# Kernel tuning notes

Measured on AMD Instinct MI355X. Metric: run time of the kernel, lower is better.

Reference implementation:

```python
import jax, jax.numpy as jnp
import numpy as np

B, S, HID = 2, 2048, 3584
NH, NKV, HD = 16, 8, 256
EPS = 1e-6
SCALING = 256 ** (-0.5)  # query_pre_attn_scalar ** -0.5
NEG = -1e9


def setup_inputs() -> dict:
    key = jax.random.key(0)
    ks = jax.random.split(key, 8)
    hidden_states = jax.random.normal(ks[0], (B, S, HID), jnp.float32)
    # RoPE tables (theta=10000), shape [B, S, HD]
    inv_freq = 1.0 / (10000.0 ** (np.arange(0, HD, 2, dtype=np.float32) / HD))
    pos = np.arange(S, dtype=np.float32)
    freqs = np.outer(pos, inv_freq)                      # [S, HD/2]
    emb = np.concatenate([freqs, freqs], axis=-1)        # [S, HD]
    cos = jnp.broadcast_to(jnp.asarray(np.cos(emb)), (B, S, HD)).astype(jnp.float32)
    sin = jnp.broadcast_to(jnp.asarray(np.sin(emb)), (B, S, HD)).astype(jnp.float32)
    # additive causal mask [B,1,S,S]
    causal = jnp.where(jnp.tril(jnp.ones((S, S), bool)), 0.0, NEG).astype(jnp.float32)
    attention_mask = jnp.broadcast_to(causal[None, None], (B, 1, S, S))
    sc = 0.02
    Wq = jax.random.normal(ks[1], (NH * HD, HID), jnp.float32) * sc
    Wk = jax.random.normal(ks[2], (NKV * HD, HID), jnp.float32) * sc
    Wv = jax.random.normal(ks[3], (NKV * HD, HID), jnp.float32) * sc
    Wo = jax.random.normal(ks[4], (HID, NH * HD), jnp.float32) * sc
    q_norm_w = jax.random.normal(ks[5], (HD,), jnp.float32) * 0.1
    k_norm_w = jax.random.normal(ks[6], (HD,), jnp.float32) * 0.1
    return dict(hidden_states=hidden_states, cos=cos, sin=sin,
                attention_mask=attention_mask, Wq=Wq, Wk=Wk, Wv=Wv, Wo=Wo,
                q_norm_w=q_norm_w, k_norm_w=k_norm_w)


def _rmsnorm(x, w, eps=EPS):
    # out = x * rsqrt(mean(x^2)) * (1 + w)
    xf = x.astype(jnp.float32)
    out = xf * jax.lax.rsqrt(jnp.mean(xf * xf, axis=-1, keepdims=True) + eps)
    return (out * (1.0 + w.astype(jnp.float32))).astype(x.dtype)


def _rotate_half(x):
    d = x.shape[-1] // 2
    return jnp.concatenate([-x[..., d:], x[..., :d]], axis=-1)


def reference(hidden_states, cos, sin, attention_mask, Wq, Wk, Wv, Wo, q_norm_w, k_norm_w):
    b, s, _ = hidden_states.shape
    # projections -> [B, H, S, D]
    q = jnp.einsum('bsh,dh->bsd', hidden_states, Wq).reshape(b, s, NH, HD).transpose(0, 2, 1, 3)
    k = jnp.einsum('bsh,dh->bsd', hidden_states, Wk).reshape(b, s, NKV, HD).transpose(0, 2, 1, 3)
    v = jnp.einsum('bsh,dh->bsd', hidden_states, Wv).reshape(b, s, NKV, HD).transpose(0, 2, 1, 3)
    # per-head RMSNorm on Q/K
    q = _rmsnorm(q, q_norm_w)
    k = _rmsnorm(k, k_norm_w)
    # RoPE, cos/sin broadcast over head dim (unsqueeze_dim=1)
    c, sn = cos[:, None], sin[:, None]
    q = q * c + _rotate_half(q) * sn
    k = k * c + _rotate_half(k) * sn
    # GQA: repeat kv heads (n_rep = NH // NKV)
    n_rep = NH // NKV
    k = jnp.repeat(k, n_rep, axis=1)
    v = jnp.repeat(v, n_rep, axis=1)
    # scaled dot-product attention, softmax in fp32
    scores = jnp.einsum('bhqd,bhkd->bhqk', q, k) * SCALING
    scores = scores + attention_mask[:, :, :, :k.shape[2]]
    attn_weights = jax.nn.softmax(scores.astype(jnp.float32), axis=-1).astype(q.dtype)
    attn_out = jnp.einsum('bhqk,bhkd->bqhd', attn_weights, v).reshape(b, s, NH * HD)
    attn_out = jnp.einsum('bsd,hd->bsh', attn_out, Wo)
    return attn_out, attn_weights
```

## Files before the change

kernel.cpp:

```cpp
#include <hip/hip_runtime.h>

#define B_    2
#define S_    2048
#define HID_  3584
#define NH_   16
#define NKV_  8
#define HD_   256
#define DQ_   (NH_ * HD_)
#define DKV_  (NKV_ * HD_)

static constexpr float SCALE_ = 0.0625f;

typedef __bf16 bf16_t;
typedef __bf16 bf16x8 __attribute__((ext_vector_type(8)));
typedef __bf16 bf16x4 __attribute__((ext_vector_type(4)));
typedef float  f32x4  __attribute__((ext_vector_type(4)));

__global__ __launch_bounds__(256) void cvt_kernel(const float* __restrict__ in,
                                                  bf16_t* __restrict__ out, int n4) {
  int i = blockIdx.x * 256 + threadIdx.x;
  if (i < n4) {
    float4 v = ((const float4*)in)[i];
    bf16x4 o;
    o[0] = (bf16_t)v.x; o[1] = (bf16_t)v.y; o[2] = (bf16_t)v.z; o[3] = (bf16_t)v.w;
    ((bf16x4*)out)[i] = o;
  }
}

__device__ inline void gload_lds16(const bf16_t* g, bf16_t* l) {
  __builtin_amdgcn_global_load_lds(
      (const __attribute__((address_space(1))) void*)g,
      (__attribute__((address_space(3))) void*)l, 16, 0, 0);
}

template<int MODE>
__global__ __launch_bounds__(512, 1) void gemm256(const bf16_t* __restrict__ A,
                                                  const bf16_t* __restrict__ Bt,
                                                  void* __restrict__ outv,
                                                  void* __restrict__ out2v,
                                                  int M, int N, int K, int nh) {
  __shared__ __align__(16) bf16_t As[2][256 * 64];
  __shared__ __align__(16) bf16_t Bs[2][256 * 64];
  const int t = threadIdx.x;
  const int lane = t & 63, wv = t >> 6;
  const int wr = wv >> 2, wc = wv & 3;
  const int lr = lane & 15, lg = lane >> 4;
  const size_t m0 = (size_t)blockIdx.y * 256, n0 = (size_t)blockIdx.x * 256;

  const int srow = wv * 8 + (lane >> 3);
  const int scol = ((lane & 7) ^ ((lane >> 3) & 7)) * 8;
  const bf16_t* ga = A  + (m0 + srow) * (size_t)K + scol;
  const bf16_t* gb = Bt + (n0 + srow) * (size_t)K + scol;
  const int ldso = wv * 512;

#define SITEA(rb, kc, pp) gload_lds16(ga + (size_t)(rb) * K + (kc), &As[pp][(rb) * 64 + ldso])
#define SITEB(rb, kc, pp) gload_lds16(gb + (size_t)(rb) * K + (kc), &Bs[pp][(rb) * 64 + ldso])

  const int NT = K >> 6;
  f32x4 acc[8][4] = {};
  bf16x8 af[4][2], bfr[2][2];

  const int swz0 = ((0 + lg) ^ (lr & 7)) * 8;
  const int swz1 = ((4 + lg) ^ (lr & 7)) * 8;
  const int aRB = (wr * 128 + lr) * 64;
  const int bRB = (wc * 64 + lr) * 64;

  SITEA(0, 0, 0); SITEA(64, 0, 0); SITEA(128, 0, 0); SITEA(192, 0, 0);
  SITEB(0, 0, 0); SITEB(64, 0, 0); SITEB(128, 0, 0); SITEB(192, 0, 0);

  for (int kt = 0; kt < NT; ++kt) {
    const int p = kt & 1, q = p ^ 1;
    __syncthreads();
    if (kt + 1 < NT) {
      const int kn = (kt + 1) << 6;
      SITEA(0, kn, q); SITEA(64, kn, q); SITEA(128, kn, q); SITEA(192, kn, q);
      SITEB(0, kn, q); SITEB(64, kn, q); SITEB(128, kn, q); SITEB(192, kn, q);
    }

#pragma unroll
    for (int i = 0; i < 4; ++i) {
      af[i][0] = *(const bf16x8*)&As[p][aRB + i * 1024 + swz0];
      af[i][1] = *(const bf16x8*)&As[p][aRB + i * 1024 + swz1];
    }
#pragma unroll
    for (int j = 0; j < 2; ++j) {
      bfr[j][0] = *(const bf16x8*)&Bs[p][bRB + j * 1024 + swz0];
      bfr[j][1] = *(const bf16x8*)&Bs[p][bRB + j * 1024 + swz1];
    }
#pragma unroll
    for (int i = 0; i < 4; ++i)
#pragma unroll
      for (int j = 0; j < 2; ++j) {
        acc[i][j] = __builtin_amdgcn_mfma_f32_16x16x32_bf16(af[i][0], bfr[j][0], acc[i][j], 0, 0, 0);
        acc[i][j] = __builtin_amdgcn_mfma_f32_16x16x32_bf16(af[i][1], bfr[j][1], acc[i][j], 0, 0, 0);
      }

#pragma unroll
    for (int i = 0; i < 4; ++i) {
      af[i][0] = *(const bf16x8*)&As[p][aRB + (i + 4) * 1024 + swz0];
      af[i][1] = *(const bf16x8*)&As[p][aRB + (i + 4) * 1024 + swz1];
    }
#pragma unroll
    for (int i = 0; i < 4; ++i)
#pragma unroll
      for (int j = 0; j < 2; ++j) {
        acc[i + 4][j] = __builtin_amdgcn_mfma_f32_16x16x32_bf16(af[i][0], bfr[j][0], acc[i + 4][j], 0, 0, 0);
        acc[i + 4][j] = __builtin_amdgcn_mfma_f32_16x16x32_bf16(af[i][1], bfr[j][1], acc[i + 4][j], 0, 0, 0);
      }

#pragma unroll
    for (int j = 0; j < 2; ++j) {
      bfr[j][0] = *(const bf16x8*)&Bs[p][bRB + (j + 2) * 1024 + swz0];
      bfr[j][1] = *(const bf16x8*)&Bs[p][bRB + (j + 2) * 1024 + swz1];
    }
#pragma unroll
    for (int i = 0; i < 4; ++i)
#pragma unroll
      for (int j = 0; j < 2; ++j) {
        acc[i + 4][j + 2] = __builtin_amdgcn_mfma_f32_16x16x32_bf16(af[i][0], bfr[j][0], acc[i + 4][j + 2], 0, 0, 0);
        acc[i + 4][j + 2] = __builtin_amdgcn_mfma_f32_16x16x32_bf16(af[i][1], bfr[j][1], acc[i + 4][j + 2], 0, 0, 0);
      }

#pragma unroll
    for (int i = 0; i < 4; ++i) {
      af[i][0] = *(const bf16x8*)&As[p][aRB + i * 1024 + swz0];
      af[i][1] = *(const bf16x8*)&As[p][aRB + i * 1024 + swz1];
    }
#pragma unroll
    for (int i = 0; i < 4; ++i)
#pragma unroll
      for (int j = 0; j < 2; ++j) {
        acc[i][j + 2] = __builtin_amdgcn_mfma_f32_16x16x32_bf16(af[i][0], bfr[j][0], acc[i][j + 2], 0, 0, 0);
        acc[i][j + 2] = __builtin_amdgcn_mfma_f32_16x16x32_bf16(af[i][1], bfr[j][1], acc[i][j + 2], 0, 0, 0);
      }
  }
#undef SITEA
#undef SITEB

#pragma unroll
  for (int i = 0; i < 8; ++i)
#pragma unroll
    for (int j = 0; j < 4; ++j) {
      const int row0 = (int)m0 + wr * 128 + i * 16 + lg * 4;
      const int col  = (int)n0 + wc * 64 + j * 16 + lr;
#pragma unroll
      for (int r = 0; r < 4; ++r) {
        const int row = row0 + r;
        if (MODE == 0) {
          ((float*)outv)[(size_t)row * N + col] = acc[i][j][r];
        } else {
          const bf16_t val = (bf16_t)acc[i][j][r];
          const int b = row >> 11, s = row & (S_ - 1);
          if (MODE == 1) {
            const int h = col >> 8, hd = col & (HD_ - 1);
            ((bf16_t*)outv)[((size_t)(b * nh + h) * S_ + s) * HD_ + hd] = val;
          } else {
            if (col < DKV_) {
              const int h = col >> 8, hd = col & (HD_ - 1);
              ((bf16_t*)outv)[((size_t)(b * NKV_ + h) * S_ + s) * HD_ + hd] = val;
            } else {
              const int c2 = col - DKV_;
              const int h = c2 >> 8, hd = c2 & (HD_ - 1);
              ((bf16_t*)out2v)[((size_t)(b * NKV_ + h) * HD_ + hd) * S_ + s] = val;
            }
          }
        }
      }
    }
}

template<int LOGNH>
__global__ __launch_bounds__(256) void normrope_kernel(bf16_t* __restrict__ x,
                                                       const float* __restrict__ w,
                                                       const float* __restrict__ cosb,
                                                       const float* __restrict__ sinb,
                                                       float* __restrict__ rownorm) {
  const int gid  = blockIdx.x * 4 + (threadIdx.x >> 6);
  const int lane = threadIdx.x & 63;
  const int nh = 1 << LOGNH;
  const int h  = gid & (nh - 1);
  const int bs = gid >> LOGNH;
  const int b  = bs >> 11, s = bs & (S_ - 1);
  const int rowi = (b * nh + h) * S_ + s;

  bf16_t* ptr = x + (size_t)rowi * HD_ + lane * 4;
  bf16x4 xv = *(const bf16x4*)ptr;
  float v0 = (float)xv[0], v1 = (float)xv[1], v2 = (float)xv[2], v3 = (float)xv[3];
  float ss = v0 * v0 + v1 * v1 + v2 * v2 + v3 * v3;
#pragma unroll
  for (int off = 1; off < 64; off <<= 1) ss += __shfl_xor(ss, off);
  float r = rsqrtf(ss * (1.0f / HD_) + 1e-6f);

  float4 wv = *(const float4*)(w + lane * 4);
  float x0 = v0 * r * (1.0f + wv.x);
  float x1 = v1 * r * (1.0f + wv.y);
  float x2 = v2 * r * (1.0f + wv.z);
  float x3 = v3 * r * (1.0f + wv.w);

  if (rownorm != nullptr) {
    float s2 = x0 * x0 + x1 * x1 + x2 * x2 + x3 * x3;
#pragma unroll
    for (int off = 1; off < 64; off <<= 1) s2 += __shfl_xor(s2, off);
    if (lane == 0) rownorm[rowi] = s2;
  }

  float p0 = __shfl_xor(x0, 32);
  float p1 = __shfl_xor(x1, 32);
  float p2 = __shfl_xor(x2, 32);
  float p3 = __shfl_xor(x3, 32);
  float sgn = (lane < 32) ? -1.0f : 1.0f;

  float4 c  = *(const float4*)(cosb + (size_t)bs * HD_ + lane * 4);
  float4 sn = *(const float4*)(sinb + (size_t)bs * HD_ + lane * 4);
  bf16x4 o;
  o[0] = (bf16_t)(x0 * c.x + sgn * p0 * sn.x);
  o[1] = (bf16_t)(x1 * c.y + sgn * p1 * sn.y);
  o[2] = (bf16_t)(x2 * c.z + sgn * p2 * sn.z);
  o[3] = (bf16_t)(x3 * c.w + sgn * p3 * sn.w);
  *(bf16x4*)ptr = o;
}

__global__ __launch_bounds__(256) void kmax_reduce_kernel(const float* __restrict__ knorm,
                                                          float* __restrict__ km) {
  __shared__ float red[4];
  const int t = threadIdx.x;
  const float* src = knorm + (size_t)blockIdx.x * S_;
  float m = 0.0f;
  for (int i = t; i < S_; i += 256) m = fmaxf(m, src[i]);
#pragma unroll
  for (int off = 1; off < 64; off <<= 1) m = fmaxf(m, __shfl_xor(m, off));
  if ((t & 63) == 0) red[t >> 6] = m;
  __syncthreads();
  if (t == 0) km[blockIdx.x] = fmaxf(fmaxf(red[0], red[1]), fmaxf(red[2], red[3]));
}

__global__ __launch_bounds__(256) void attn1p_kernel(const bf16_t* __restrict__ qb,
                                                     const bf16_t* __restrict__ kb,
                                                     const bf16_t* __restrict__ vt,
                                                     const float* __restrict__ kmaxbuf,
                                                     bf16_t* __restrict__ pt,
                                                     float* __restrict__ linv,
                                                     bf16_t* __restrict__ ctx) {
  __shared__ __align__(16) bf16_t Ks[32][264];
  __shared__ __align__(16) bf16_t Vs[256][36];
  __shared__ __align__(16) bf16_t p_lds[4][16][36];
  __shared__ float qn_lds[4][16];

  const int t = threadIdx.x, w = t >> 6, lane = t & 63;
  const int lr = lane & 15, lg = lane >> 4, rloc = lg * 4;

  const int wgid = blockIdx.x;
  const int g    = ((wgid >> 9) << 3) | (wgid & 7);
  const int idx  = (wgid >> 3) & 63;
  const int b    = g >> 3, kvh = g & 7;
  const int h    = kvh * 2 + (idx >> 5);
  const int qbucket = 31 - (idx & 31);
  const int bh   = b * NH_ + h;
  const int q0b  = qbucket * 64;
  const int q0   = q0b + w * 16;

  const bf16_t* qptr = qb + ((size_t)bh * S_ + q0 + lr) * HD_ + lg * 8;
  bf16x8 qf[8];
#pragma unroll
  for (int c = 0; c < 8; ++c) qf[c] = *(const bf16x8*)(qptr + c * 32);

  float qn = 0.0f;
#pragma unroll
  for (int c = 0; c < 8; ++c)
#pragma unroll
    for (int e = 0; e < 8; ++e) { float v = (float)qf[c][e]; qn += v * v; }
  qn += __shfl_xor(qn, 16);
  qn += __shfl_xor(qn, 32);
  if (lg == 0) qn_lds[w][lr] = qn;
  __syncthreads();
  const float kmax2 = kmaxbuf[b * NKV_ + kvh];
  float mb[4];
#pragma unroll
  for (int r = 0; r < 4; ++r)
    mb[r] = SCALE_ * sqrtf(qn_lds[w][rloc + r] * kmax2) + 1.0f;

  float l[4] = {0.f, 0.f, 0.f, 0.f};
  f32x4 oacc[16] = {};
  const int nkt = (q0b + 64) >> 5;
  bf16_t* prow_g = pt + ((size_t)bh * S_ + q0) * S_;
  const bf16_t* kgb = kb + (size_t)(b * NKV_ + kvh) * S_ * HD_;
  const bf16_t* vgb = vt + (size_t)(b * NKV_ + kvh) * HD_ * S_;

  const int s_st = t >> 3, c_st = (t & 7) * 32;
  const int vd   = t >> 3, vc   = (t & 7) * 4;
  const int prow = lane >> 2, pcol = (lane & 3) * 8;

  bf16x8 kreg0, kreg1, kreg2, kreg3;
  bf16x4 vreg[8];
  {
    const bf16_t* src = kgb + (size_t)s_st * HD_ + c_st;
    kreg0 = *(const bf16x8*)(src);
    kreg1 = *(const bf16x8*)(src + 8);
    kreg2 = *(const bf16x8*)(src + 16);
    kreg3 = *(const bf16x8*)(src + 24);
#pragma unroll
    for (int i = 0; i < 8; ++i)
      vreg[i] = *(const bf16x4*)(vgb + (size_t)(vd + i * 32) * S_ + vc);
  }

  for (int kt = 0; kt < nkt; ++kt) {
    const int colb = kt * 32;
    __syncthreads();
    *(bf16x8*)&Ks[s_st][c_st]      = kreg0;
    *(bf16x8*)&Ks[s_st][c_st + 8]  = kreg1;
    *(bf16x8*)&Ks[s_st][c_st + 16] = kreg2;
    *(bf16x8*)&Ks[s_st][c_st + 24] = kreg3;
#pragma unroll
    for (int i = 0; i < 8; ++i) *(bf16x4*)&Vs[vd + i * 32][vc] = vreg[i];
    __syncthreads();

    if (kt + 1 < nkt) {
      const int nb = colb + 32;
      const bf16_t* src = kgb + (size_t)(nb + s_st) * HD_ + c_st;
      kreg0 = *(const bf16x8*)(src);
      kreg1 = *(const bf16x8*)(src + 8);
      kreg2 = *(const bf16x8*)(src + 16);
      kreg3 = *(const bf16x8*)(src + 24);
#pragma unroll
      for (int i = 0; i < 8; ++i)
        vreg[i] = *(const bf16x4*)(vgb + (size_t)(vd + i * 32) * S_ + nb + vc);
    }

    if (colb <= q0 + 15) {
      f32x4 s0 = {0.f, 0.f, 0.f, 0.f}, s1 = {0.f, 0.f, 0.f, 0.f};
#pragma unroll
      for (int c = 0; c < 8; ++c) {
        bf16x8 k0 = *(const bf16x8*)&Ks[lr][c * 32 + lg * 8];
        bf16x8 k1 = *(const bf16x8*)&Ks[16 + lr][c * 32 + lg * 8];
        s0 = __builtin_amdgcn_mfma_f32_16x16x32_bf16(qf[c], k0, s0, 0, 0, 0);
        s1 = __builtin_amdgcn_mfma_f32_16x16x32_bf16(qf[c], k1, s1, 0, 0, 0);
      }
      const int col0 = colb + lr, col1 = col0 + 16;
#pragma unroll
      for (int r = 0; r < 4; ++r) {
        const int row = q0 + rloc + r;
        const float pa = (col0 <= row) ? __expf(s0[r] * SCALE_ - mb[r]) : 0.0f;
        const float pb = (col1 <= row) ? __expf(s1[r] * SCALE_ - mb[r]) : 0.0f;
        l[r] += pa + pb;
        p_lds[w][rloc + r][lr]      = (bf16_t)pa;
        p_lds[w][rloc + r][lr + 16] = (bf16_t)pb;
      }
      bf16x8 pf = *(const bf16x8*)&p_lds[w][lr][lg * 8];
#pragma unroll
      for (int df = 0; df < 16; ++df) {
        bf16x8 vf = *(const bf16x8*)&Vs[df * 16 + lr][lg * 8];
        oacc[df] = __builtin_amdgcn_mfma_f32_16x16x32_bf16(pf, vf, oacc[df], 0, 0, 0);
      }
      {
        bf16x8 pv = *(const bf16x8*)&p_lds[w][prow][pcol];
        *(bf16x8*)(prow_g + (size_t)prow * S_ + colb + pcol) = pv;
      }
    }
  }
#pragma unroll
  for (int r = 0; r < 4; ++r) {
    l[r] += __shfl_xor(l[r], 1);
    l[r] += __shfl_xor(l[r], 2);
    l[r] += __shfl_xor(l[r], 4);
    l[r] += __shfl_xor(l[r], 8);
  }
  float invl[4];
#pragma unroll
  for (int r = 0; r < 4; ++r) invl[r] = 1.0f / l[r];

  bf16_t* cp = ctx + ((size_t)b * S_ + q0) * DQ_ + h * HD_;
#pragma unroll
  for (int df = 0; df < 16; ++df)
#pragma unroll
    for (int r = 0; r < 4; ++r)
      cp[(size_t)(rloc + r) * DQ_ + df * 16 + lr] = (bf16_t)(oacc[df][r] * invl[r]);

  if (lr == 0) {
#pragma unroll
    for (int r = 0; r < 4; ++r) linv[(size_t)bh * S_ + q0 + rloc + r] = invl[r];
  }
}

__global__ __launch_bounds__(256) void wscale_kernel(float* __restrict__ wbuf,
                                                     const bf16_t* __restrict__ pt,
                                                     const float* __restrict__ linv) {
  const int wv = threadIdx.x >> 6, lane = threadIdx.x & 63;
  const size_t rg = (size_t)blockIdx.x * 4 + wv;
  const int row = (int)(rg & (S_ - 1));
  const float inv = linv[rg];
  const bf16_t* src = pt + rg * S_;
  float* base = wbuf + rg * S_;
#pragma unroll
  for (int i = 0; i < 8; ++i) {
    const int c0 = (i * 64 + lane) * 4;
    float4 v;
    if (c0 > row) {
      v = make_float4(0.f, 0.f, 0.f, 0.f);
    } else {
      bf16x4 bv = *(const bf16x4*)(src + c0);
      v.x = (c0 + 0 <= row) ? (float)bv[0] * inv : 0.f;
      v.y = (c0 + 1 <= row) ? (float)bv[1] * inv : 0.f;
      v.z = (c0 + 2 <= row) ? (float)bv[2] * inv : 0.f;
      v.w = (c0 + 3 <= row) ? (float)bv[3] * inv : 0.f;
    }
    *(float4*)(base + c0) = v;
  }
}

extern "C" void kernel_launch(void* const* d_in, const int* in_sizes, int n_in,
                              void* d_out, int out_size, void* d_ws, size_t ws_size,
                              hipStream_t stream) {
  const float* hs   = (const float*)d_in[0];
  const float* cosb = (const float*)d_in[1];
  const float* sinb = (const float*)d_in[2];
  const float* Wq = (const float*)d_in[4];
  const float* Wk = (const float*)d_in[5];
  const float* Wv = (const float*)d_in[6];
  const float* Wo = (const float*)d_in[7];
  const float* qw = (const float*)d_in[8];
  const float* kw = (const float*)d_in[9];

  char* ws = (char*)d_ws;
  bf16_t* qb    = (bf16_t*)(ws + 0);
  bf16_t* kb    = (bf16_t*)(ws + 33554432);
  bf16_t* vt    = (bf16_t*)(ws + 50331648);
  bf16_t* ctx   = (bf16_t*)(ws + 67108864);
  float*  linv  = (float*)(ws + 100663296);
  float*  knorm = (float*)(ws + 100925440);
  float*  km    = (float*)(ws + 101056512);
  bf16_t* hsb   = (bf16_t*)(ws + 101056640);
  bf16_t* wqb   = (bf16_t*)(ws + 130416768);
  bf16_t* wkb   = (bf16_t*)(ws + 159776896);
  bf16_t* wvb   = (bf16_t*)(ws + 174456960);
  bf16_t* wob   = (bf16_t*)(ws + 189137024);
  bf16_t* pt    = (bf16_t*)(ws + 218497152);

  float* out      = (float*)d_out;
  float* attn_out = out;
  float* weights  = out + (size_t)B_ * S_ * HID_;

  const int M = B_ * S_;

  cvt_kernel<<<14336, 256, 0, stream>>>(hs, hsb, (B_ * S_ * HID_) / 4);
  cvt_kernel<<<14336, 256, 0, stream>>>(Wq, wqb, (DQ_ * HID_) / 4);
  cvt_kernel<<<7168,  256, 0, stream>>>(Wk, wkb, (DKV_ * HID_) / 4);
  cvt_kernel<<<7168,  256, 0, stream>>>(Wv, wvb, (DKV_ * HID_) / 4);
  cvt_kernel<<<14336, 256, 0, stream>>>(Wo, wob, (HID_ * DQ_) / 4);

  gemm256<1><<<dim3(DQ_ / 256, M / 256), 512, 0, stream>>>(hsb, wqb, qb, nullptr, M, DQ_, HID_, NH_);
  gemm256<3><<<dim3((2 * DKV_) / 256, M / 256), 512, 0, stream>>>(hsb, wkb, kb, vt, M, 2 * DKV_, HID_, NKV_);

  normrope_kernel<4><<<(B_ * S_ * NH_) / 4, 256, 0, stream>>>(qb, qw, cosb, sinb, nullptr);
  normrope_kernel<3><<<(B_ * S_ * NKV_) / 4, 256, 0, stream>>>(kb, kw, cosb, sinb, knorm);
  kmax_reduce_kernel<<<B_ * NKV_, 256, 0, stream>>>(knorm, km);

  attn1p_kernel<<<(S_ / 64) * (B_ * NH_), 256, 0, stream>>>(qb, kb, vt, km, pt, linv, ctx);

  wscale_kernel<<<(B_ * NH_ * S_) / 4, 256, 0, stream>>>(weights, pt, linv);

  gemm256<0><<<dim3(HID_ / 256, M / 256), 512, 0, stream>>>(ctx, wob, attn_out, nullptr, M, HID_, DQ_, 0);
}
```

Measured before the change: 870.0 us.

## Fuse Q/K/V projections into one GEMM and merge norm-rope kernels

```diff
diff --git a/kernel.cpp b/kernel.cpp
--- a/kernel.cpp
+++ b/kernel.cpp
@@ -38,7 +38,8 @@
                                                   const bf16_t* __restrict__ Bt,
                                                   void* __restrict__ outv,
                                                   void* __restrict__ out2v,
-                                                  int M, int N, int K, int nh) {
+                                                  void* __restrict__ out3v,
+                                                  int M, int N, int K) {
   __shared__ __align__(16) bf16_t As[2][256 * 64];
   __shared__ __align__(16) bf16_t Bs[2][256 * 64];
   const int t = threadIdx.x;
@@ -151,35 +152,39 @@
         } else {
           const bf16_t val = (bf16_t)acc[i][j][r];
           const int b = row >> 11, s = row & (S_ - 1);
-          if (MODE == 1) {
+          if (col < DQ_) {
             const int h = col >> 8, hd = col & (HD_ - 1);
-            ((bf16_t*)outv)[((size_t)(b * nh + h) * S_ + s) * HD_ + hd] = val;
+            ((bf16_t*)outv)[((size_t)(b * NH_ + h) * S_ + s) * HD_ + hd] = val;
+          } else if (col < DQ_ + DKV_) {
+            const int c2 = col - DQ_;
+            const int h = c2 >> 8, hd = c2 & (HD_ - 1);
+            ((bf16_t*)out2v)[((size_t)(b * NKV_ + h) * S_ + s) * HD_ + hd] = val;
           } else {
-            if (col < DKV_) {
-              const int h = col >> 8, hd = col & (HD_ - 1);
-              ((bf16_t*)outv)[((size_t)(b * NKV_ + h) * S_ + s) * HD_ + hd] = val;
-            } else {
-              const int c2 = col - DKV_;
-              const int h = c2 >> 8, hd = c2 & (HD_ - 1);
-              ((bf16_t*)out2v)[((size_t)(b * NKV_ + h) * HD_ + hd) * S_ + s] = val;
-            }
+            const int c2 = col - DQ_ - DKV_;
+            const int h = c2 >> 8, hd = c2 & (HD_ - 1);
+            ((bf16_t*)out3v)[((size_t)(b * NKV_ + h) * HD_ + hd) * S_ + s] = val;
           }
         }
       }
     }
 }
 
-template<int LOGNH>
-__global__ __launch_bounds__(256) void normrope_kernel(bf16_t* __restrict__ x,
-                                                       const float* __restrict__ w,
-                                                       const float* __restrict__ cosb,
-                                                       const float* __restrict__ sinb,
-                                                       float* __restrict__ rownorm) {
-  const int gid  = blockIdx.x * 4 + (threadIdx.x >> 6);
+__global__ __launch_bounds__(256) void normrope2_kernel(bf16_t* __restrict__ qb,
+                                                        bf16_t* __restrict__ kb,
+                                                        const float* __restrict__ qw,
+                                                        const float* __restrict__ kw,
+                                                        const float* __restrict__ cosb,
+                                                        const float* __restrict__ sinb,
+                                                        float* __restrict__ qnorm,
+                                                        float* __restrict__ knorm) {
+  int gid = blockIdx.x * 4 + (threadIdx.x >> 6);
   const int lane = threadIdx.x & 63;
-  const int nh = 1 << LOGNH;
+  bf16_t* x; const float* w; float* rn; int lognh;
+  if (gid < B_ * S_ * NH_) { x = qb; w = qw; rn = qnorm; lognh = 4; }
+  else { gid -= B_ * S_ * NH_; x = kb; w = kw; rn = knorm; lognh = 3; }
+  const int nh = 1 << lognh;
   const int h  = gid & (nh - 1);
-  const int bs = gid >> LOGNH;
+  const int bs = gid >> lognh;
   const int b  = bs >> 11, s = bs & (S_ - 1);
   const int rowi = (b * nh + h) * S_ + s;
 
@@ -197,12 +202,10 @@
   float x2 = v2 * r * (1.0f + wv.z);
   float x3 = v3 * r * (1.0f + wv.w);
 
-  if (rownorm != nullptr) {
-    float s2 = x0 * x0 + x1 * x1 + x2 * x2 + x3 * x3;
-#pragma unroll
-    for (int off = 1; off < 64; off <<= 1) s2 += __shfl_xor(s2, off);
-    if (lane == 0) rownorm[rowi] = s2;
-  }
+  float s2 = x0 * x0 + x1 * x1 + x2 * x2 + x3 * x3;
+#pragma unroll
+  for (int off = 1; off < 64; off <<= 1) s2 += __shfl_xor(s2, off);
+  if (lane == 0) rn[rowi] = s2;
 
   float p0 = __shfl_xor(x0, 32);
   float p1 = __shfl_xor(x1, 32);
@@ -237,6 +240,7 @@
 __global__ __launch_bounds__(256) void attn1p_kernel(const bf16_t* __restrict__ qb,
                                                      const bf16_t* __restrict__ kb,
                                                      const bf16_t* __restrict__ vt,
+                                                     const float* __restrict__ qnorm,
                                                      const float* __restrict__ kmaxbuf,
                                                      bf16_t* __restrict__ pt,
                                                      float* __restrict__ linv,
@@ -244,7 +248,6 @@
   __shared__ __align__(16) bf16_t Ks[32][264];
   __shared__ __align__(16) bf16_t Vs[256][36];
   __shared__ __align__(16) bf16_t p_lds[4][16][36];
-  __shared__ float qn_lds[4][16];
 
   const int t = threadIdx.x, w = t >> 6, lane = t & 63;
   const int lr = lane & 15, lg = lane >> 4, rloc = lg * 4;
@@ -264,20 +267,11 @@
 #pragma unroll
   for (int c = 0; c < 8; ++c) qf[c] = *(const bf16x8*)(qptr + c * 32);
 
-  float qn = 0.0f;
-#pragma unroll
-  for (int c = 0; c < 8; ++c)
-#pragma unroll
-    for (int e = 0; e < 8; ++e) { float v = (float)qf[c][e]; qn += v * v; }
-  qn += __shfl_xor(qn, 16);
-  qn += __shfl_xor(qn, 32);
-  if (lg == 0) qn_lds[w][lr] = qn;
-  __syncthreads();
   const float kmax2 = kmaxbuf[b * NKV_ + kvh];
   float mb[4];
 #pragma unroll
   for (int r = 0; r < 4; ++r)
-    mb[r] = SCALE_ * sqrtf(qn_lds[w][rloc + r] * kmax2) + 1.0f;
+    mb[r] = SCALE_ * sqrtf(qnorm[(size_t)bh * S_ + q0 + rloc + r] * kmax2) + 1.0f;
 
   float l[4] = {0.f, 0.f, 0.f, 0.f};
   f32x4 oacc[16] = {};
@@ -434,6 +428,7 @@
   bf16_t* wvb   = (bf16_t*)(ws + 174456960);
   bf16_t* wob   = (bf16_t*)(ws + 189137024);
   bf16_t* pt    = (bf16_t*)(ws + 218497152);
+  float*  qnorm = (float*)(ws + 486932608);
 
   float* out      = (float*)d_out;
   float* attn_out = out;
@@ -447,16 +442,17 @@
   cvt_kernel<<<7168,  256, 0, stream>>>(Wv, wvb, (DKV_ * HID_) / 4);
   cvt_kernel<<<14336, 256, 0, stream>>>(Wo, wob, (HID_ * DQ_) / 4);
 
-  gemm256<1><<<dim3(DQ_ / 256, M / 256), 512, 0, stream>>>(hsb, wqb, qb, nullptr, M, DQ_, HID_, NH_);
-  gemm256<3><<<dim3((2 * DKV_) / 256, M / 256), 512, 0, stream>>>(hsb, wkb, kb, vt, M, 2 * DKV_, HID_, NKV_);
-
-  normrope_kernel<4><<<(B_ * S_ * NH_) / 4, 256, 0, stream>>>(qb, qw, cosb, sinb, nullptr);
-  normrope_kernel<3><<<(B_ * S_ * NKV_) / 4, 256, 0, stream>>>(kb, kw, cosb, sinb, knorm);
+  gemm256<4><<<dim3((DQ_ + 2 * DKV_) / 256, M / 256), 512, 0, stream>>>(
+      hsb, wqb, qb, kb, vt, M, DQ_ + 2 * DKV_, HID_);
+
+  normrope2_kernel<<<(B_ * S_ * (NH_ + NKV_)) / 4, 256, 0, stream>>>(
+      qb, kb, qw, kw, cosb, sinb, qnorm, knorm);
   kmax_reduce_kernel<<<B_ * NKV_, 256, 0, stream>>>(knorm, km);
 
-  attn1p_kernel<<<(S_ / 64) * (B_ * NH_), 256, 0, stream>>>(qb, kb, vt, km, pt, linv, ctx);
+  attn1p_kernel<<<(S_ / 64) * (B_ * NH_), 256, 0, stream>>>(qb, kb, vt, qnorm, km, pt, linv, ctx);
 
   wscale_kernel<<<(B_ * NH_ * S_) / 4, 256, 0, stream>>>(weights, pt, linv);
 
-  gemm256<0><<<dim3(HID_ / 256, M / 256), 512, 0, stream>>>(ctx, wob, attn_out, nullptr, M, HID_, DQ_, 0);
-}
+  gemm256<0><<<dim3(HID_ / 256, M / 256), 512, 0, stream>>>(
+      ctx, wob, attn_out, nullptr, nullptr, M, HID_, DQ_);
+}
```

After: 906.2 us. 1.04x slower.
